# Kernel tuning notes

Hardware: AMD Instinct MI355X
Metric: run time of the kernel (lower is better)

Reference implementation:

```python
import math
import jax, jax.numpy as jnp
import numpy as np

GRID = 16          # img_size // patch_size = 224 // 14
N_PER_H = 2048     # n_neurons // n_head = 8192 // 4
THETA = 10000.0


def _freqs_2d():
    """2D RoPE phase table, shape (1, 1, GRID*GRID, N_PER_H).
    Layout per position: [h_phases | w_phases | h_phases | w_phases], each half_dim//2 wide.
    """
    dim = N_PER_H
    half = dim // 2
    inv_freq = 1.0 / THETA ** (jnp.arange(0, half, 2, dtype=jnp.float32) / half)  # (half//2,)
    pos = jnp.arange(GRID, dtype=jnp.float32)
    ph = pos[:, None] * inv_freq[None, :]                       # (GRID, half//2)
    ph_h = jnp.broadcast_to(ph[:, None, :], (GRID, GRID, half // 2))
    ph_w = jnp.broadcast_to(ph[None, :, :], (GRID, GRID, half // 2))
    phases = jnp.concatenate([ph_h, ph_w, ph_h, ph_w], axis=-1)  # (GRID, GRID, dim)
    return phases.reshape(1, 1, GRID * GRID, dim)


def _rope(phases, v):
    ang = (phases % 1.0) * (2.0 * math.pi)
    c = jnp.cos(ang)
    s = jnp.sin(ang)
    # interleaved rotation: (-v_odd, v_even) re-interleaved
    v_rot = jnp.stack((-v[..., 1::2], v[..., ::2]), axis=-1).reshape(v.shape)
    return (v * c).astype(v.dtype) + (v_rot * s).astype(v.dtype)


def setup_inputs() -> dict:
    key = jax.random.key(0)
    kq, kk, kv = jax.random.split(key, 3)
    B, H, T, N = 16, 4, 256, N_PER_H
    D = 256
    Q = jax.random.normal(kq, (B, H, T, N), dtype=jnp.float32)
    K = jax.random.normal(kk, (B, H, T, N), dtype=jnp.float32)
    V = jax.random.normal(kv, (B, 1, T, D), dtype=jnp.float32)
    return {"Q": Q, "K": K, "V": V}


def reference(Q, K, V):
    B, H, T, N = Q.shape
    n_patches = GRID * GRID
    freqs = _freqs_2d()[:, :, :n_patches, :N]
    if T == n_patches + 1:  # static-shape branch (CLS token)
        Qr = jnp.concatenate([Q[:, :, :1, :], _rope(freqs, Q[:, :, 1:, :])], axis=2)
        Kr = jnp.concatenate([K[:, :, :1, :], _rope(freqs, K[:, :, 1:, :])], axis=2)
    else:
        f = freqs[:, :, :T, :]
        Qr = _rope(f, Q)
        Kr = _rope(f, K)
    # non-softmax bidirectional attention
    scores = jnp.einsum('bhtn,bhsn->bhts', Qr, Kr) / math.sqrt(N)  # (B,H,T,T)
    return jnp.matmul(scores, V)  # V (B,1,T,D) broadcasts over H -> (B,H,T,D)
```

## Files before the change

### kernel.cpp

```cpp
#include <hip/hip_runtime.h>
#include <hip/hip_bf16.h>

#define T_  256
#define NN_ 2048

typedef short bf16x8 __attribute__((ext_vector_type(8)));
typedef float f32x4  __attribute__((ext_vector_type(4)));

__device__ __forceinline__ unsigned short f2bf(float x) {
    union { float f; unsigned u; } v; v.f = x;
    unsigned r = v.u + 0x7fffu + ((v.u >> 16) & 1u);
    return (unsigned short)(r >> 16);
}

__device__ __forceinline__ float bflo(unsigned w) {
    union { unsigned u; float f; } v; v.u = w << 16; return v.f;
}
__device__ __forceinline__ float bfhi(unsigned w) {
    union { unsigned u; float f; } v; v.u = w & 0xffff0000u; return v.f;
}
__device__ __forceinline__ unsigned pkbf(float lo, float hi) {
    union { __hip_bfloat16 h; unsigned short s; } a, b;
    a.h = __float2bfloat16(lo);
    b.h = __float2bfloat16(hi);
    return (unsigned)a.s | ((unsigned)b.s << 16);
}

__global__ void build_cs(unsigned* __restrict__ cs) {
    int idx = blockIdx.x * 256 + threadIdx.x;
    int p = idx >> 9, f = idx & 511;
    float inv = powf(10000.0f, -(float)f * (1.0f / 512.0f));
    float ph  = (float)p * inv;
    float ang = (ph - floorf(ph)) * 6.28318530717958647692f;
    float s, c;
    sincosf(ang, &s, &c);
    cs[idx] = pkbf(c, s);
}

__launch_bounds__(256, 2)
__global__ void gemm1(const float* __restrict__ Q, const float* __restrict__ K,
                      const unsigned* __restrict__ cs, unsigned short* __restrict__ scores) {
    __shared__ __align__(16) unsigned short Als[2][128 * 72];
    __shared__ __align__(16) unsigned short Bls[2][64 * 72];

    const int tid  = threadIdx.x;
    const int bh   = blockIdx.x & 63;
    const int tile = blockIdx.x >> 6;
    const int ti = (tile >> 2) << 7;
    const int si = (tile & 3) << 6;

    const float* Qb = Q + (size_t)bh * (T_ * NN_);
    const float* Kb = K + (size_t)bh * (T_ * NN_);

    const float* qpA[4]; int cshA[4], cswA[4], ldsA[4];
    const float* qpB[2]; int cshB[2], cswB[2], ldsB[2];
#pragma unroll
    for (int i = 0; i < 4; i++) {
        int lin = i * 256 + tid;
        int row = lin >> 3, c8 = (lin & 7) << 3;
        int gr = ti + row;
        qpA[i]  = Qb + (size_t)gr * NN_ + c8;
        cshA[i] = ((gr >> 4) << 9) + c8;
        cswA[i] = ((gr & 15) << 9) + c8;
        ldsA[i] = row * 72 + c8;
    }
#pragma unroll
    for (int i = 0; i < 2; i++) {
        int lin = i * 256 + tid;
        int row = lin >> 3, c8 = (lin & 7) << 3;
        int gr = si + row;
        qpB[i]  = Kb + (size_t)gr * NN_ + c8;
        cshB[i] = ((gr >> 4) << 9) + c8;
        cswB[i] = ((gr & 15) << 9) + c8;
        ldsB[i] = row * 72 + c8;
    }

    const int wv = tid >> 6, lane = tid & 63;
    const int lr = lane & 15, lg = lane >> 4;
    const int m0 = (wv >> 1) * 64;
    const int n0 = (wv & 1) * 32;

    f32x4 acc[4][2];
#pragma unroll
    for (int i = 0; i < 4; i++)
#pragma unroll
        for (int j = 0; j < 2; j++) acc[i][j] = (f32x4){0.f, 0.f, 0.f, 0.f};

    auto LOAD = [&](float4 (&a)[8], float4 (&b)[4], int k0) {
#pragma unroll
        for (int i = 0; i < 4; i++) {
            a[2*i]   = *(const float4*)(qpA[i] + k0);
            a[2*i+1] = *(const float4*)(qpA[i] + k0 + 4);
        }
#pragma unroll
        for (int i = 0; i < 2; i++) {
            b[2*i]   = *(const float4*)(qpB[i] + k0);
            b[2*i+1] = *(const float4*)(qpB[i] + k0 + 4);
        }
    };

    auto WRITE = [&](int buf, const float4 (&a)[8], const float4 (&b)[4], int k0) {
        const int fk = k0 & 511;
        const int w  = (k0 >> 9) & 1;
#pragma unroll
        for (int i = 0; i < 4; i++) {
            int off = (w ? cswA[i] : cshA[i]) + fk;
            uint4 u0 = *(const uint4*)(cs + off);
            uint4 u1 = *(const uint4*)(cs + off + 4);
            float4 f0 = a[2*i], f1 = a[2*i+1];
            uint4 o;
            o.x = pkbf(f0.x*bflo(u0.x) - f0.y*bfhi(u0.x),
                       f0.y*bflo(u0.y) + f0.x*bfhi(u0.y));
            o.y = pkbf(f0.z*bflo(u0.z) - f0.w*bfhi(u0.z),
                       f0.w*bflo(u0.w) + f0.z*bfhi(u0.w));
            o.z = pkbf(f1.x*bflo(u1.x) - f1.y*bfhi(u1.x),
                       f1.y*bflo(u1.y) + f1.x*bfhi(u1.y));
            o.w = pkbf(f1.z*bflo(u1.z) - f1.w*bfhi(u1.z),
                       f1.w*bflo(u1.w) + f1.z*bfhi(u1.w));
            *(uint4*)(&Als[buf][ldsA[i]]) = o;
        }
#pragma unroll
        for (int i = 0; i < 2; i++) {
            int off = (w ? cswB[i] : cshB[i]) + fk;
            uint4 u0 = *(const uint4*)(cs + off);
            uint4 u1 = *(const uint4*)(cs + off + 4);
            float4 f0 = b[2*i], f1 = b[2*i+1];
            uint4 o;
            o.x = pkbf(f0.x*bflo(u0.x) - f0.y*bfhi(u0.x),
                       f0.y*bflo(u0.y) + f0.x*bfhi(u0.y));
            o.y = pkbf(f0.z*bflo(u0.z) - f0.w*bfhi(u0.z),
                       f0.w*bflo(u0.w) + f0.z*bfhi(u0.w));
            o.z = pkbf(f1.x*bflo(u1.x) - f1.y*bfhi(u1.x),
                       f1.y*bflo(u1.y) + f1.x*bfhi(u1.y));
            o.w = pkbf(f1.z*bflo(u1.z) - f1.w*bfhi(u1.z),
                       f1.w*bflo(u1.w) + f1.z*bfhi(u1.w));
            *(uint4*)(&Bls[buf][ldsB[i]]) = o;
        }
    };

    auto COMPUTE = [&](int buf) {
#pragma unroll
        for (int kk = 0; kk < 64; kk += 32) {
            bf16x8 af[4], bfr[2];
#pragma unroll
            for (int mi = 0; mi < 4; mi++)
                af[mi] = *(const bf16x8*)(&Als[buf][(m0 + mi * 16 + lr) * 72 + kk + lg * 8]);
#pragma unroll
            for (int ni = 0; ni < 2; ni++)
                bfr[ni] = *(const bf16x8*)(&Bls[buf][(n0 + ni * 16 + lr) * 72 + kk + lg * 8]);
#pragma unroll
            for (int mi = 0; mi < 4; mi++)
#pragma unroll
                for (int ni = 0; ni < 2; ni++)
                    acc[mi][ni] = __builtin_amdgcn_mfma_f32_16x16x32_bf16(
                        af[mi], bfr[ni], acc[mi][ni], 0, 0, 0);
        }
    };

    auto BAR = [&]() {
        asm volatile("s_waitcnt lgkmcnt(0)" ::: "memory");
        __builtin_amdgcn_s_barrier();
        asm volatile("" ::: "memory");
    };

    float4 a0[8], a1[8], b0[4], b1[4];

    LOAD(a0, b0, 0);
    LOAD(a1, b1, 64);
    WRITE(0, a0, b0, 0);
    BAR();

    for (int t2 = 0; t2 < 15; t2++) {
        const int t = t2 * 2;
        LOAD(a0, b0, (t + 2) * 64);
        COMPUTE(0);
        WRITE(1, a1, b1, (t + 1) * 64);
        BAR();
        LOAD(a1, b1, (t + 3) * 64);
        COMPUTE(1);
        WRITE(0, a0, b0, (t + 2) * 64);
        BAR();
    }
    COMPUTE(0);
    WRITE(1, a1, b1, 31 * 64);
    BAR();
    COMPUTE(1);

    const float rs = 0.02209708691207961f;
    unsigned short* sb = scores + (size_t)bh * (T_ * T_);
#pragma unroll
    for (int mi = 0; mi < 4; mi++) {
        int tr = ti + m0 + mi * 16 + lg * 4;
#pragma unroll
        for (int ni = 0; ni < 2; ni++) {
            int sc = si + n0 + ni * 16 + lr;
#pragma unroll
            for (int r = 0; r < 4; r++)
                sb[(size_t)(tr + r) * 256 + sc] = f2bf(acc[mi][ni][r] * rs);
        }
    }
}

__launch_bounds__(512)
__global__ void gemm2(const unsigned short* __restrict__ scores,
                      const float* __restrict__ V, float* __restrict__ out) {
    __shared__ __align__(16) unsigned short Als[2][128 * 72];
    __shared__ __align__(16) unsigned short Bls[2][128 * 72];

    const int tid  = threadIdx.x;
    const int bh   = blockIdx.x >> 2;
    const int b    = bh >> 2;
    const int tile = blockIdx.x & 3;
    const int ti = (tile >> 1) << 7;
    const int d0 = (tile & 1) << 7;

    const unsigned short* Sb = scores + (size_t)bh * (256 * 256);
    const float* Vb = V + (size_t)b * (256 * 256);

    const int wv = tid >> 6, lane = tid & 63;
    const int lr = lane & 15, lg = lane >> 4;
    const int m0 = (wv >> 2) * 64;
    const int n0 = (wv & 3) * 32;

    f32x4 acc[4][2];
#pragma unroll
    for (int i = 0; i < 4; i++)
#pragma unroll
        for (int j = 0; j < 2; j++) acc[i][j] = (f32x4){0.f, 0.f, 0.f, 0.f};

    uint4 sA[2]; float4 vB[4];

    auto LOAD = [&](int k0) {
#pragma unroll
        for (int i = 0; i < 2; i++) {
            int lin = i * 512 + tid;
            int row = lin >> 3;
            int c8  = (lin & 7) << 3;
            sA[i] = *(const uint4*)(Sb + (size_t)(ti + row) * 256 + k0 + c8);
        }
#pragma unroll
        for (int i = 0; i < 4; i++) {
            int lin  = i * 512 + tid;
            int srow = lin >> 5;
            int c4   = (lin & 31) << 2;
            vB[i] = *(const float4*)(Vb + (size_t)(k0 + srow) * 256 + d0 + c4);
        }
    };

    auto WRITE = [&](int buf) {
#pragma unroll
        for (int i = 0; i < 2; i++) {
            int lin = i * 512 + tid;
            int row = lin >> 3;
            int c8  = (lin & 7) << 3;
            *(uint4*)(&Als[buf][row * 72 + c8]) = sA[i];
        }
#pragma unroll
        for (int i = 0; i < 4; i++) {
            int lin  = i * 512 + tid;
            int srow = lin >> 5;
            int c4   = (lin & 31) << 2;
            Bls[buf][(c4 + 0) * 72 + srow] = f2bf(vB[i].x);
            Bls[buf][(c4 + 1) * 72 + srow] = f2bf(vB[i].y);
            Bls[buf][(c4 + 2) * 72 + srow] = f2bf(vB[i].z);
            Bls[buf][(c4 + 3) * 72 + srow] = f2bf(vB[i].w);
        }
    };

    auto COMPUTE = [&](int buf) {
#pragma unroll
        for (int kk = 0; kk < 64; kk += 32) {
            bf16x8 af[4], bfr[2];
#pragma unroll
            for (int mi = 0; mi < 4; mi++)
                af[mi] = *(const bf16x8*)(&Als[buf][(m0 + mi * 16 + lr) * 72 + kk + lg * 8]);
#pragma unroll
            for (int ni = 0; ni < 2; ni++)
                bfr[ni] = *(const bf16x8*)(&Bls[buf][(n0 + ni * 16 + lr) * 72 + kk + lg * 8]);
#pragma unroll
            for (int mi = 0; mi < 4; mi++)
#pragma unroll
                for (int ni = 0; ni < 2; ni++)
                    acc[mi][ni] = __builtin_amdgcn_mfma_f32_16x16x32_bf16(
                        af[mi], bfr[ni], acc[mi][ni], 0, 0, 0);
        }
    };

    LOAD(0);
    WRITE(0);
    __syncthreads();

    int cur = 0;
    for (int t = 0; t < 3; t++) {
        LOAD((t + 1) * 64);
        COMPUTE(cur);
        WRITE(cur ^ 1);
        __syncthreads();
        cur ^= 1;
    }
    COMPUTE(cur);

    float* ob = out + (size_t)bh * (256 * 256);
#pragma unroll
    for (int mi = 0; mi < 4; mi++) {
        int tr = ti + m0 + mi * 16 + lg * 4;
#pragma unroll
        for (int ni = 0; ni < 2; ni++) {
            int dc = d0 + n0 + ni * 16 + lr;
#pragma unroll
            for (int r = 0; r < 4; r++)
                ob[(size_t)(tr + r) * 256 + dc] = acc[mi][ni][r];
        }
    }
}

extern "C" void kernel_launch(void* const* d_in, const int* in_sizes, int n_in,
                              void* d_out, int out_size, void* d_ws, size_t ws_size,
                              hipStream_t stream) {
    const float* Q = (const float*)d_in[0];
    const float* K = (const float*)d_in[1];
    const float* V = (const float*)d_in[2];
    float* out = (float*)d_out;

    unsigned* cs = (unsigned*)d_ws;
    unsigned short* scores = (unsigned short*)((char*)d_ws + 32768);

    build_cs<<<dim3(32), dim3(256), 0, stream>>>(cs);
    gemm1<<<dim3(512), dim3(256), 0, stream>>>(Q, K, cs, scores);
    gemm2<<<dim3(256), dim3(512), 0, stream>>>(scores, V, out);
}
```

Baseline: 155.9 us.

## Pre-transpose V to bf16, regrid gemm1/gemm2 waves, prefetch cos/sin table

```diff
diff --git a/kernel.cpp b/kernel.cpp
--- a/kernel.cpp
+++ b/kernel.cpp
@@ -12,7 +12,6 @@
     unsigned r = v.u + 0x7fffu + ((v.u >> 16) & 1u);
     return (unsigned short)(r >> 16);
 }
-
 __device__ __forceinline__ float bflo(unsigned w) {
     union { unsigned u; float f; } v; v.u = w << 16; return v.f;
 }
@@ -37,7 +36,38 @@
     cs[idx] = pkbf(c, s);
 }
 
-__launch_bounds__(256, 2)
+__global__ void vtrans(const float* __restrict__ V, unsigned short* __restrict__ Vt) {
+    __shared__ unsigned short Tl[64 * 72];
+    const int tid = threadIdx.x;
+    const int b  = blockIdx.x >> 4;
+    const int s0 = ((blockIdx.x >> 2) & 3) << 6;
+    const int d0 = (blockIdx.x & 3) << 6;
+    const float* Vb = V + (size_t)b * 65536;
+#pragma unroll
+    for (int u = 0; u < 4; u++) {
+        int lin = u * 256 + tid;
+        int srow = lin >> 4, c4 = (lin & 15) << 2;
+        float4 v = *(const float4*)(Vb + (size_t)(s0 + srow) * 256 + d0 + c4);
+        Tl[(c4 + 0) * 72 + srow] = f2bf(v.x);
+        Tl[(c4 + 1) * 72 + srow] = f2bf(v.y);
+        Tl[(c4 + 2) * 72 + srow] = f2bf(v.z);
+        Tl[(c4 + 3) * 72 + srow] = f2bf(v.w);
+    }
+    __syncthreads();
+    unsigned short* Vtb = Vt + (size_t)b * 65536;
+#pragma unroll
+    for (int u = 0; u < 2; u++) {
+        int lin = u * 256 + tid;
+        int drow = lin >> 3, sc8 = (lin & 7) << 3;
+        *(uint4*)(Vtb + (size_t)(d0 + drow) * 256 + s0 + sc8) =
+            *(const uint4*)(&Tl[drow * 72 + sc8]);
+    }
+}
+
+struct QKSet { float4 a[4]; float4 b[2]; };
+struct CSet  { uint4  a[4]; uint4  b[2]; };
+
+__launch_bounds__(512, 4)
 __global__ void gemm1(const float* __restrict__ Q, const float* __restrict__ K,
                       const unsigned* __restrict__ cs, unsigned short* __restrict__ scores) {
     __shared__ __align__(16) unsigned short Als[2][128 * 72];
@@ -52,28 +82,167 @@
     const float* Qb = Q + (size_t)bh * (T_ * NN_);
     const float* Kb = K + (size_t)bh * (T_ * NN_);
 
-    const float* qpA[4]; int cshA[4], cswA[4], ldsA[4];
-    const float* qpB[2]; int cshB[2], cswB[2], ldsB[2];
-#pragma unroll
-    for (int i = 0; i < 4; i++) {
-        int lin = i * 256 + tid;
+    const float* qpA[2]; int cshA[2], cswA[2], ldsA[2];
+    const float* qpB0;   int cshB0,  cswB0,  ldsB0;
+#pragma unroll
+    for (int u = 0; u < 2; u++) {
+        int lin = u * 512 + tid;
         int row = lin >> 3, c8 = (lin & 7) << 3;
         int gr = ti + row;
-        qpA[i]  = Qb + (size_t)gr * NN_ + c8;
-        cshA[i] = ((gr >> 4) << 9) + c8;
-        cswA[i] = ((gr & 15) << 9) + c8;
-        ldsA[i] = row * 72 + c8;
-    }
-#pragma unroll
-    for (int i = 0; i < 2; i++) {
-        int lin = i * 256 + tid;
-        int row = lin >> 3, c8 = (lin & 7) << 3;
+        qpA[u]  = Qb + (size_t)gr * NN_ + c8;
+        cshA[u] = ((gr >> 4) << 9) + c8;
+        cswA[u] = ((gr & 15) << 9) + c8;
+        ldsA[u] = row * 72 + c8;
+    }
+    {
+        int row = tid >> 3, c8 = (tid & 7) << 3;
         int gr = si + row;
-        qpB[i]  = Kb + (size_t)gr * NN_ + c8;
-        cshB[i] = ((gr >> 4) << 9) + c8;
-        cswB[i] = ((gr & 15) << 9) + c8;
-        ldsB[i] = row * 72 + c8;
-    }
+        qpB0  = Kb + (size_t)gr * NN_ + c8;
+        cshB0 = ((gr >> 4) << 9) + c8;
+        cswB0 = ((gr & 15) << 9) + c8;
+        ldsB0 = row * 72 + c8;
+    }
+
+    const int wv = tid >> 6, lane = tid & 63;
+    const int lr = lane & 15, lg = lane >> 4;
+    const int m0 = (wv >> 1) << 5;
+    const int n0 = (wv & 1) << 5;
+
+    f32x4 acc[2][2];
+#pragma unroll
+    for (int i = 0; i < 2; i++)
+#pragma unroll
+        for (int j = 0; j < 2; j++) acc[i][j] = (f32x4){0.f, 0.f, 0.f, 0.f};
+
+    auto LOAD = [&](QKSet& s, int k0) {
+#pragma unroll
+        for (int u = 0; u < 2; u++) {
+            s.a[2*u]   = *(const float4*)(qpA[u] + k0);
+            s.a[2*u+1] = *(const float4*)(qpA[u] + k0 + 4);
+        }
+        s.b[0] = *(const float4*)(qpB0 + k0);
+        s.b[1] = *(const float4*)(qpB0 + k0 + 4);
+    };
+
+    auto CSLOAD = [&](CSet& c, int k0) {
+        const int fk = k0 & 511;
+        const int w  = (k0 >> 9) & 1;
+#pragma unroll
+        for (int u = 0; u < 2; u++) {
+            const unsigned* p = cs + (w ? cswA[u] : cshA[u]) + fk;
+            c.a[2*u]   = *(const uint4*)(p);
+            c.a[2*u+1] = *(const uint4*)(p + 4);
+        }
+        const unsigned* p = cs + (w ? cswB0 : cshB0) + fk;
+        c.b[0] = *(const uint4*)(p);
+        c.b[1] = *(const uint4*)(p + 4);
+    };
+
+    auto ROT = [&](const float4& f0, const float4& f1,
+                   const uint4& u0, const uint4& u1) -> uint4 {
+        uint4 o;
+        o.x = pkbf(f0.x*bflo(u0.x) - f0.y*bfhi(u0.x),
+                   f0.y*bflo(u0.y) + f0.x*bfhi(u0.y));
+        o.y = pkbf(f0.z*bflo(u0.z) - f0.w*bfhi(u0.z),
+                   f0.w*bflo(u0.w) + f0.z*bfhi(u0.w));
+        o.z = pkbf(f1.x*bflo(u1.x) - f1.y*bfhi(u1.x),
+                   f1.y*bflo(u1.y) + f1.x*bfhi(u1.y));
+        o.w = pkbf(f1.z*bflo(u1.z) - f1.w*bfhi(u1.z),
+                   f1.w*bflo(u1.w) + f1.z*bfhi(u1.w));
+        return o;
+    };
+
+    auto WRITE = [&](int buf, const QKSet& s, const CSet& c) {
+#pragma unroll
+        for (int u = 0; u < 2; u++)
+            *(uint4*)(&Als[buf][ldsA[u]]) = ROT(s.a[2*u], s.a[2*u+1], c.a[2*u], c.a[2*u+1]);
+        *(uint4*)(&Bls[buf][ldsB0]) = ROT(s.b[0], s.b[1], c.b[0], c.b[1]);
+    };
+
+    auto COMPUTE = [&](int buf) {
+        __builtin_amdgcn_s_setprio(1);
+#pragma unroll
+        for (int kk = 0; kk < 64; kk += 32) {
+            bf16x8 af[2], bfr[2];
+#pragma unroll
+            for (int mi = 0; mi < 2; mi++)
+                af[mi] = *(const bf16x8*)(&Als[buf][(m0 + mi * 16 + lr) * 72 + kk + lg * 8]);
+#pragma unroll
+            for (int ni = 0; ni < 2; ni++)
+                bfr[ni] = *(const bf16x8*)(&Bls[buf][(n0 + ni * 16 + lr) * 72 + kk + lg * 8]);
+#pragma unroll
+            for (int mi = 0; mi < 2; mi++)
+#pragma unroll
+                for (int ni = 0; ni < 2; ni++)
+                    acc[mi][ni] = __builtin_amdgcn_mfma_f32_16x16x32_bf16(
+                        af[mi], bfr[ni], acc[mi][ni], 0, 0, 0);
+        }
+        __builtin_amdgcn_s_setprio(0);
+    };
+
+    auto BAR = [&]() {
+        asm volatile("s_waitcnt lgkmcnt(0)" ::: "memory");
+        __builtin_amdgcn_s_barrier();
+        asm volatile("" ::: "memory");
+    };
+
+    QKSet s0, s1; CSet c;
+
+    LOAD(s0, 0);
+    LOAD(s1, 64);
+    CSLOAD(c, 0);
+    WRITE(0, s0, c);
+    CSLOAD(c, 64);
+    BAR();
+
+    for (int t2 = 0; t2 < 15; t2++) {
+        const int t = t2 * 2;
+        LOAD(s0, (t + 2) * 64);
+        COMPUTE(0);
+        WRITE(1, s1, c);
+        CSLOAD(c, (t + 2) * 64);
+        BAR();
+        LOAD(s1, (t + 3) * 64);
+        COMPUTE(1);
+        WRITE(0, s0, c);
+        CSLOAD(c, (t + 3) * 64);
+        BAR();
+    }
+    COMPUTE(0);
+    WRITE(1, s1, c);
+    BAR();
+    COMPUTE(1);
+
+    const float rs = 0.02209708691207961f;
+    unsigned short* sb = scores + (size_t)bh * (T_ * T_);
+#pragma unroll
+    for (int mi = 0; mi < 2; mi++) {
+        int tr = ti + m0 + mi * 16 + lg * 4;
+#pragma unroll
+        for (int ni = 0; ni < 2; ni++) {
+            int sc = si + n0 + ni * 16 + lr;
+#pragma unroll
+            for (int r = 0; r < 4; r++)
+                sb[(size_t)(tr + r) * 256 + sc] = f2bf(acc[mi][ni][r] * rs);
+        }
+    }
+}
+
+__launch_bounds__(256, 2)
+__global__ void gemm2(const unsigned short* __restrict__ scores,
+                      const unsigned short* __restrict__ Vt, float* __restrict__ out) {
+    __shared__ __align__(16) unsigned short Als[2][128 * 72];
+    __shared__ __align__(16) unsigned short Bls[2][64 * 72];
+
+    const int tid  = threadIdx.x;
+    const int bh   = blockIdx.x & 63;
+    const int b    = bh >> 2;
+    const int tile = blockIdx.x >> 6;
+    const int ti = (tile >> 2) << 7;
+    const int d0 = (tile & 3) << 6;
+
+    const unsigned short* Sb  = scores + (size_t)bh * 65536;
+    const unsigned short* Vtb = Vt + (size_t)b * 65536;
 
     const int wv = tid >> 6, lane = tid & 63;
     const int lr = lane & 15, lg = lane >> 4;
@@ -86,59 +255,40 @@
 #pragma unroll
         for (int j = 0; j < 2; j++) acc[i][j] = (f32x4){0.f, 0.f, 0.f, 0.f};
 
-    auto LOAD = [&](float4 (&a)[8], float4 (&b)[4], int k0) {
-#pragma unroll
-        for (int i = 0; i < 4; i++) {
-            a[2*i]   = *(const float4*)(qpA[i] + k0);
-            a[2*i+1] = *(const float4*)(qpA[i] + k0 + 4);
-        }
-#pragma unroll
-        for (int i = 0; i < 2; i++) {
-            b[2*i]   = *(const float4*)(qpB[i] + k0);
-            b[2*i+1] = *(const float4*)(qpB[i] + k0 + 4);
-        }
-    };
-
-    auto WRITE = [&](int buf, const float4 (&a)[8], const float4 (&b)[4], int k0) {
-        const int fk = k0 & 511;
-        const int w  = (k0 >> 9) & 1;
-#pragma unroll
-        for (int i = 0; i < 4; i++) {
-            int off = (w ? cswA[i] : cshA[i]) + fk;
-            uint4 u0 = *(const uint4*)(cs + off);
-            uint4 u1 = *(const uint4*)(cs + off + 4);
-            float4 f0 = a[2*i], f1 = a[2*i+1];
-            uint4 o;
-            o.x = pkbf(f0.x*bflo(u0.x) - f0.y*bfhi(u0.x),
-                       f0.y*bflo(u0.y) + f0.x*bfhi(u0.y));
-            o.y = pkbf(f0.z*bflo(u0.z) - f0.w*bfhi(u0.z),
-                       f0.w*bflo(u0.w) + f0.z*bfhi(u0.w));
-            o.z = pkbf(f1.x*bflo(u1.x) - f1.y*bfhi(u1.x),
-                       f1.y*bflo(u1.y) + f1.x*bfhi(u1.y));
-            o.w = pkbf(f1.z*bflo(u1.z) - f1.w*bfhi(u1.z),
-                       f1.w*bflo(u1.w) + f1.z*bfhi(u1.w));
-            *(uint4*)(&Als[buf][ldsA[i]]) = o;
-        }
-#pragma unroll
-        for (int i = 0; i < 2; i++) {
-            int off = (w ? cswB[i] : cshB[i]) + fk;
-            uint4 u0 = *(const uint4*)(cs + off);
-            uint4 u1 = *(const uint4*)(cs + off + 4);
-            float4 f0 = b[2*i], f1 = b[2*i+1];
-            uint4 o;
-            o.x = pkbf(f0.x*bflo(u0.x) - f0.y*bfhi(u0.x),
-                       f0.y*bflo(u0.y) + f0.x*bfhi(u0.y));
-            o.y = pkbf(f0.z*bflo(u0.z) - f0.w*bfhi(u0.z),
-                       f0.w*bflo(u0.w) + f0.z*bfhi(u0.w));
-            o.z = pkbf(f1.x*bflo(u1.x) - f1.y*bfhi(u1.x),
-                       f1.y*bflo(u1.y) + f1.x*bfhi(u1.y));
-            o.w = pkbf(f1.z*bflo(u1.z) - f1.w*bfhi(u1.z),
-                       f1.w*bflo(u1.w) + f1.z*bfhi(u1.w));
-            *(uint4*)(&Bls[buf][ldsB[i]]) = o;
+    uint4 sA[4], sB[2];
+
+    auto LOAD = [&](int k0) {
+#pragma unroll
+        for (int u = 0; u < 4; u++) {
+            int lin = u * 256 + tid;
+            int row = lin >> 3, c8 = (lin & 7) << 3;
+            sA[u] = *(const uint4*)(Sb + (size_t)(ti + row) * 256 + k0 + c8);
+        }
+#pragma unroll
+        for (int u = 0; u < 2; u++) {
+            int lin = u * 256 + tid;
+            int row = lin >> 3, c8 = (lin & 7) << 3;
+            sB[u] = *(const uint4*)(Vtb + (size_t)(d0 + row) * 256 + k0 + c8);
+        }
+    };
+
+    auto WRITE = [&](int buf) {
+#pragma unroll
+        for (int u = 0; u < 4; u++) {
+            int lin = u * 256 + tid;
+            int row = lin >> 3, c8 = (lin & 7) << 3;
+            *(uint4*)(&Als[buf][row * 72 + c8]) = sA[u];
+        }
+#pragma unroll
+        for (int u = 0; u < 2; u++) {
+            int lin = u * 256 + tid;
+            int row = lin >> 3, c8 = (lin & 7) << 3;
+            *(uint4*)(&Bls[buf][row * 72 + c8]) = sB[u];
         }
     };
 
     auto COMPUTE = [&](int buf) {
+        __builtin_amdgcn_s_setprio(1);
 #pragma unroll
         for (int kk = 0; kk < 64; kk += 32) {
             bf16x8 af[4], bfr[2];
@@ -155,6 +305,7 @@
                     acc[mi][ni] = __builtin_amdgcn_mfma_f32_16x16x32_bf16(
                         af[mi], bfr[ni], acc[mi][ni], 0, 0, 0);
         }
+        __builtin_amdgcn_s_setprio(0);
     };
 
     auto BAR = [&]() {
@@ -163,144 +314,21 @@
         asm volatile("" ::: "memory");
     };
 
-    float4 a0[8], a1[8], b0[4], b1[4];
-
-    LOAD(a0, b0, 0);
-    LOAD(a1, b1, 64);
-    WRITE(0, a0, b0, 0);
-    BAR();
-
-    for (int t2 = 0; t2 < 15; t2++) {
-        const int t = t2 * 2;
-        LOAD(a0, b0, (t + 2) * 64);
-        COMPUTE(0);
-        WRITE(1, a1, b1, (t + 1) * 64);
-        BAR();
-        LOAD(a1, b1, (t + 3) * 64);
-        COMPUTE(1);
-        WRITE(0, a0, b0, (t + 2) * 64);
-        BAR();
-    }
-    COMPUTE(0);
-    WRITE(1, a1, b1, 31 * 64);
-    BAR();
-    COMPUTE(1);
-
-    const float rs = 0.02209708691207961f;
-    unsigned short* sb = scores + (size_t)bh * (T_ * T_);
-#pragma unroll
-    for (int mi = 0; mi < 4; mi++) {
-        int tr = ti + m0 + mi * 16 + lg * 4;
-#pragma unroll
-        for (int ni = 0; ni < 2; ni++) {
-            int sc = si + n0 + ni * 16 + lr;
-#pragma unroll
-            for (int r = 0; r < 4; r++)
-                sb[(size_t)(tr + r) * 256 + sc] = f2bf(acc[mi][ni][r] * rs);
-        }
-    }
-}
-
-__launch_bounds__(512)
-__global__ void gemm2(const unsigned short* __restrict__ scores,
-                      const float* __restrict__ V, float* __restrict__ out) {
-    __shared__ __align__(16) unsigned short Als[2][128 * 72];
-    __shared__ __align__(16) unsigned short Bls[2][128 * 72];
-
-    const int tid  = threadIdx.x;
-    const int bh   = blockIdx.x >> 2;
-    const int b    = bh >> 2;
-    const int tile = blockIdx.x & 3;
-    const int ti = (tile >> 1) << 7;
-    const int d0 = (tile & 1) << 7;
-
-    const unsigned short* Sb = scores + (size_t)bh * (256 * 256);
-    const float* Vb = V + (size_t)b * (256 * 256);
-
-    const int wv = tid >> 6, lane = tid & 63;
-    const int lr = lane & 15, lg = lane >> 4;
-    const int m0 = (wv >> 2) * 64;
-    const int n0 = (wv & 3) * 32;
-
-    f32x4 acc[4][2];
-#pragma unroll
-    for (int i = 0; i < 4; i++)
-#pragma unroll
-        for (int j = 0; j < 2; j++) acc[i][j] = (f32x4){0.f, 0.f, 0.f, 0.f};
-
-    uint4 sA[2]; float4 vB[4];
-
-    auto LOAD = [&](int k0) {
-#pragma unroll
-        for (int i = 0; i < 2; i++) {
-            int lin = i * 512 + tid;
-            int row = lin >> 3;
-            int c8  = (lin & 7) << 3;
-            sA[i] = *(const uint4*)(Sb + (size_t)(ti + row) * 256 + k0 + c8);
-        }
-#pragma unroll
-        for (int i = 0; i < 4; i++) {
-            int lin  = i * 512 + tid;
-            int srow = lin >> 5;
-            int c4   = (lin & 31) << 2;
-            vB[i] = *(const float4*)(Vb + (size_t)(k0 + srow) * 256 + d0 + c4);
-        }
-    };
-
-    auto WRITE = [&](int buf) {
-#pragma unroll
-        for (int i = 0; i < 2; i++) {
-            int lin = i * 512 + tid;
-            int row = lin >> 3;
-            int c8  = (lin & 7) << 3;
-            *(uint4*)(&Als[buf][row * 72 + c8]) = sA[i];
-        }
-#pragma unroll
-        for (int i = 0; i < 4; i++) {
-            int lin  = i * 512 + tid;
-            int srow = lin >> 5;
-            int c4   = (lin & 31) << 2;
-            Bls[buf][(c4 + 0) * 72 + srow] = f2bf(vB[i].x);
-            Bls[buf][(c4 + 1) * 72 + srow] = f2bf(vB[i].y);
-            Bls[buf][(c4 + 2) * 72 + srow] = f2bf(vB[i].z);
-            Bls[buf][(c4 + 3) * 72 + srow] = f2bf(vB[i].w);
-        }
-    };
-
-    auto COMPUTE = [&](int buf) {
-#pragma unroll
-        for (int kk = 0; kk < 64; kk += 32) {
-            bf16x8 af[4], bfr[2];
-#pragma unroll
-            for (int mi = 0; mi < 4; mi++)
-                af[mi] = *(const bf16x8*)(&Als[buf][(m0 + mi * 16 + lr) * 72 + kk + lg * 8]);
-#pragma unroll
-            for (int ni = 0; ni < 2; ni++)
-                bfr[ni] = *(const bf16x8*)(&Bls[buf][(n0 + ni * 16 + lr) * 72 + kk + lg * 8]);
-#pragma unroll
-            for (int mi = 0; mi < 4; mi++)
-#pragma unroll
-                for (int ni = 0; ni < 2; ni++)
-                    acc[mi][ni] = __builtin_amdgcn_mfma_f32_16x16x32_bf16(
-                        af[mi], bfr[ni], acc[mi][ni], 0, 0, 0);
-        }
-    };
-
     LOAD(0);
     WRITE(0);
-    __syncthreads();
+    BAR();
 
     int cur = 0;
     for (int t = 0; t < 3; t++) {
         LOAD((t + 1) * 64);
         COMPUTE(cur);
         WRITE(cur ^ 1);
-        __syncthreads();
+        BAR();
         cur ^= 1;
     }
     COMPUTE(cur);
 
-    float* ob = out + (size_t)bh * (256 * 256);
+    float* ob = out + (size_t)bh * 65536;
 #pragma unroll
     for (int mi = 0; mi < 4; mi++) {
         int tr = ti + m0 + mi * 16 + lg * 4;
@@ -324,8 +352,10 @@
 
     unsigned* cs = (unsigned*)d_ws;
     unsigned short* scores = (unsigned short*)((char*)d_ws + 32768);
+    unsigned short* Vt = (unsigned short*)((char*)d_ws + 32768 + 8388608);
 
     build_cs<<<dim3(32), dim3(256), 0, stream>>>(cs);
-    gemm1<<<dim3(512), dim3(256), 0, stream>>>(Q, K, cs, scores);
-    gemm2<<<dim3(256), dim3(512), 0, stream>>>(scores, V, out);
-}
+    vtrans<<<dim3(256), dim3(256), 0, stream>>>(V, Vt);
+    gemm1<<<dim3(512), dim3(512), 0, stream>>>(Q, K, cs, scores);
+    gemm2<<<dim3(512), dim3(256), 0, stream>>>(scores, Vt, out);
+}
```

Measured after the change: 167.6 us. 1.07x slower.
